# Performance work log

Measured on AMD Instinct MI355X. Metric: run time of the kernel, lower is better.

The kernel has to match this reference:

```python
import jax, jax.numpy as jnp
import numpy as np

B, C, S = 16, 8, 128
DT, DX, DY = 0.001, 1.0, 1.0
NUM_STEPS = 10
EPS = 1e-6


def _thomas(a, b, c, d):
    """Batched Thomas tridiagonal solve. a,b,c,d: [M,N] rows; solve along N."""
    aT, bT, cT, dT = a.T, b.T, c.T, d.T  # [N, M]
    zero = jnp.zeros_like(dT[0])

    def fwd(carry, inp):
        cs_p, ds_p = carry
        ai, bi, ci, di = inp
        denom = bi - ai * cs_p + EPS  # i=0: cs_p=0 -> denom = b0 + eps (matches torch)
        cs = ci / denom
        ds = (di - ai * ds_p) / denom
        return (cs, ds), (cs, ds)

    _, (c_star, d_star) = jax.lax.scan(fwd, (zero, zero), (aT, bT, cT, dT))

    def bwd(x_next, inp):
        ci, di = inp
        x = di - ci * x_next
        return x, x

    _, xs = jax.lax.scan(bwd, d_star[-1], (c_star[:-1], d_star[:-1]), reverse=True)
    x = jnp.concatenate([xs, d_star[-1:]], axis=0)  # [N, M]
    return x.T


def _diffuse_rows(u2d, coeff):
    """Implicit 1D diffusion along last axis. u2d, coeff: [M,N]."""
    a = -coeff
    c = -coeff
    b = 1.0 + 2.0 * coeff
    b = b.at[:, 0].set(1.0 + coeff[:, 0])
    b = b.at[:, -1].set(1.0 + coeff[:, -1])
    return _thomas(a, b, c, u2d)


def _forward(u, alpha_base, beta_base, alpha_time_coeff, beta_time_coeff, channel_mixing):
    Bb, Cc, H, W = u.shape
    half = DT / 2.0
    t = 0.0
    for _ in range(NUM_STEPS):
        # x half-step (coefficient alpha at time t)
        alpha = jnp.clip(alpha_base + alpha_time_coeff * t, EPS, 10.0)
        u = jnp.einsum('dc,bchw->bdhw', channel_mixing, u)
        uf = u.reshape(Bb * Cc, H, W)
        af = jnp.broadcast_to(alpha[None], (Bb, Cc, H, W)).reshape(Bb * Cc, H, W)
        uf = _diffuse_rows(uf.reshape(-1, W), af.reshape(-1, W) * half / DX**2).reshape(Bb * Cc, H, W)
        t += half
        # y full step (coefficient beta at time t+dt/2)
        beta = jnp.clip(beta_base + beta_time_coeff * t, EPS, 10.0)
        bf = jnp.broadcast_to(beta[None], (Bb, Cc, H, W)).reshape(Bb * Cc, H, W)
        ut = uf.transpose(0, 2, 1).reshape(-1, H)
        bt = bf.transpose(0, 2, 1).reshape(-1, H)
        ut = _diffuse_rows(ut, bt * DT / DY**2)
        uf = ut.reshape(Bb * Cc, W, H).transpose(0, 2, 1)
        t += half
        # x half-step (coefficient alpha at time t+dt)
        alpha = jnp.clip(alpha_base + alpha_time_coeff * t, EPS, 10.0)
        af = jnp.broadcast_to(alpha[None], (Bb, Cc, H, W)).reshape(Bb * Cc, H, W)
        uf = _diffuse_rows(uf.reshape(-1, W), af.reshape(-1, W) * half / DX**2).reshape(Bb * Cc, H, W)
        u = uf.reshape(Bb, Cc, H, W)
    return u


def setup_inputs() -> dict:
    key = jax.random.key(0)
    k_u, k_cm, k_atc, k_btc = jax.random.split(key, 4)
    u = jax.random.normal(k_u, (B, C, S, S), dtype=jnp.float32)
    alpha_base = jnp.ones((C, S, S), dtype=jnp.float32)
    beta_base = jnp.ones((C, S, S), dtype=jnp.float32)
    alpha_time_coeff = jax.random.normal(k_atc, (C, S, S), dtype=jnp.float32) * 0.01
    beta_time_coeff = jax.random.normal(k_btc, (C, S, S), dtype=jnp.float32) * 0.01
    channel_mixing = jnp.eye(C, dtype=jnp.float32) + jax.random.normal(k_cm, (C, C), dtype=jnp.float32) * 0.01
    return {
        'u': u,
        'alpha_base': alpha_base,
        'beta_base': beta_base,
        'alpha_time_coeff': alpha_time_coeff,
        'beta_time_coeff': beta_time_coeff,
        'channel_mixing': channel_mixing,
    }


def reference(u, alpha_base, beta_base, alpha_time_coeff, beta_time_coeff, channel_mixing):
    return _forward(u, alpha_base, beta_base, alpha_time_coeff, beta_time_coeff, channel_mixing)
```

## Files before the change

### kernel.cpp

```cpp
#include <hip/hip_runtime.h>
#include <hip/hip_fp16.h>


constexpr int S_  = 128;
constexpr int RS  = 129;
constexpr float EPSF = 1e-6f;
constexpr int CSS = 8 * 128 * 128;

constexpr int SOFF_A = 0;
constexpr int SOFF_B = 64 * 128;
constexpr int SOFF_C = 128 * 128;
constexpr int SPOOL  = 192 * 128;

__device__ __forceinline__ int swad(int r, int b) {
    return r * 128 + (((b) ^ (r & 31)) << 2);
}

template <int N>
__device__ __forceinline__ void jrunN(const float (&e)[N], const float (&g)[N],
                                      float (&o)[N - 4]) {
    float x1[N];
    #pragma unroll
    for (int i = 1; i <= N - 2; ++i) x1[i] = fmaf(g[i], e[i - 1] + e[i + 1], e[i]);
    #pragma unroll
    for (int i = 2; i <= N - 3; ++i) o[i - 2] = fmaf(g[i], x1[i - 1] + x1[i + 1], e[i]);
}

__global__ __launch_bounds__(256) void coef_kernel(
    const float* __restrict__ ab, const float* __restrict__ atc,
    const float* __restrict__ bb, const float* __restrict__ btc,
    __half2* __restrict__ cf)
{
    for (int gc = blockIdx.x * 256 + threadIdx.x; gc < CSS; gc += gridDim.x * 256) {
        const int w = gc & 127, h = (gc >> 7) & 127;
        const float abv = ab[gc], atv = atc[gc], bbv = bb[gc], btv = btc[gc];
        const float nbY = (h == 0 || h == S_ - 1) ? 1.f : 2.f;
        const float nbX = (w == 0 || w == S_ - 1) ? 1.f : 2.f;
        for (int k = 0; k < 10; ++k) {
            const float ty = (2 * k + 1) * 0.0005f;
            const float tx = (2 * k + 2) * 0.0005f;
            float be = fminf(fmaxf(fmaf(btv, ty, bbv), EPSF), 10.f);
            float co = be * 0.001f;
            float rb = __builtin_amdgcn_rcpf(fmaf(nbY, co, 1.f) + EPSF);
            cf[k * CSS + gc] = __floats2half2_rn(rb * co, rb - 1.f);
            float al = fminf(fmaxf(fmaf(atv, tx, abv), EPSF), 10.f);
            co = al * 0.0005f;
            rb = __builtin_amdgcn_rcpf(fmaf(nbX, co, 1.f) + EPSF);
            cf[(10 + k) * CSS + gc] = __floats2half2_rn(rb * co, rb - 1.f);
        }
        float al = fminf(fmaxf(abv, EPSF), 10.f);
        float co = al * 0.0005f;
        float rb = __builtin_amdgcn_rcpf(fmaf(nbX, co, 1.f) + EPSF);
        cf[20 * CSS + gc] = __floats2half2_rn(rb * co, rb - 1.f);
    }
}

__global__ __launch_bounds__(512, 2) void head_kernel(
    const float* __restrict__ u0, __half* __restrict__ ud,
    const __half2* __restrict__ cfy, const __half2* __restrict__ cfx,
    const __half2* __restrict__ cfx0, const float* __restrict__ cm)
{
    constexpr int POOL   = 288 * RS;
    constexpr int OFF_A  = 0;
    constexpr int OFF_B  = 64 * RS;
    constexpr int OFF_CP = 192 * RS;
    constexpr int OFF_X0 = 96 * RS;
    __shared__ float sP[POOL];
    const int tid = threadIdx.x;
    const int b   = blockIdx.x >> 4;
    const int h0  = (blockIdx.x & 15) << 3;

    #pragma unroll
    for (int m = 0; m < 2; ++m) {
        const int col = tid + 512 * m;
        const int c = col >> 7, w = col & 127;
        #pragma unroll
        for (int hh = 0; hh < 12; ++hh) {
            const int gh = h0 - 2 + hh;
            float v = 0.f;
            if (gh >= 0 && gh < S_) v = u0[((b * 8 + c) * S_ + gh) * S_ + w];
            sP[(c * 12 + hh) * RS + w] = v;
        }
    }
    #pragma unroll
    for (int m = 0; m < 12; ++m) {
        const int task = tid + 512 * m;
        const int r = task >> 6, col2 = task & 63;
        const int c = r / 12, hh = r % 12;
        int gh = h0 - 2 + hh; gh = gh < 0 ? 0 : (gh >= S_ ? S_ - 1 : gh);
        const uint2 v = ((const uint2*)cfx0)[(c * S_ + gh) * 64 + col2];
        sP[OFF_CP + r * RS + col2 * 2]     = __uint_as_float(v.x);
        sP[OFF_CP + r * RS + col2 * 2 + 1] = __uint_as_float(v.y);
    }
    __syncthreads();
    {
        float M[64];
        #pragma unroll
        for (int i = 0; i < 64; ++i) M[i] = cm[i];
        #pragma unroll
        for (int m = 0; m < 3; ++m) {
            const int p = tid + 512 * m;
            const int hh = p >> 7, w = p & 127;
            float v[8], o[8];
            #pragma unroll
            for (int c = 0; c < 8; ++c) v[c] = sP[(c * 12 + hh) * RS + w];
            #pragma unroll
            for (int dd = 0; dd < 8; ++dd) {
                float a = 0.f;
                #pragma unroll
                for (int c = 0; c < 8; ++c) a = fmaf(M[dd * 8 + c], v[c], a);
                o[dd] = a;
            }
            #pragma unroll
            for (int c = 0; c < 8; ++c) sP[(c * 12 + hh) * RS + w] = o[c];
        }
    }
    __syncthreads();
    #pragma unroll
    for (int m = 0; m < 3; ++m) {
        const int task = tid + 512 * m;
        const int r96 = task % 96, wr = task / 96;
        const int hh = r96 % 12;
        const int gh = h0 - 2 + hh;
        const bool rowin = (gh >= 0 && gh < S_);
        const int w0 = wr * 8;
        float e[12], g[12];
        #pragma unroll
        for (int j = 0; j < 12; ++j) {
            const int wj = w0 - 2 + j;
            const bool win = (wj >= 0 && wj < S_);
            const float dv = win ? sP[r96 * RS + wj] : 0.f;
            uint cb = (rowin && win) ? __float_as_uint(sP[OFF_CP + r96 * RS + wj]) : 0u;
            const float2 f = __half22float2(*reinterpret_cast<__half2*>(&cb));
            e[j] = (1.f + f.y) * dv;
            g[j] = f.x;
        }
        float o[8]; jrunN<12>(e, g, o);
        #pragma unroll
        for (int i = 0; i < 8; ++i) sP[OFF_X0 + r96 * RS + w0 + i] = o[i];
    }
    __syncthreads();

    #pragma unroll
    for (int m = 0; m < 2; ++m) {
        const int col = tid + 512 * m;
        const int c = col >> 7, w = col & 127;
        float e[12], g[12];
        #pragma unroll
        for (int hh = 0; hh < 12; ++hh) {
            const int gh = h0 - 2 + hh;
            const bool inr = (gh >= 0 && gh < S_);
            const int ghc = inr ? gh : 0;
            const float dv = sP[OFF_X0 + (c * 12 + hh) * RS + w];
            const float2 f = __half22float2(cfy[(c * S_ + ghc) * S_ + w]);
            e[hh] = (1.f + f.y) * dv;
            g[hh] = inr ? f.x : 0.f;
        }
        float o[8]; jrunN<12>(e, g, o);
        #pragma unroll
        for (int i = 0; i < 8; ++i) sP[OFF_A + (c * 8 + i) * RS + w] = o[i];
    }
    __syncthreads();
    #pragma unroll
    for (int m = 0; m < 8; ++m) {
        const int task = tid + 512 * m;
        const int r = task >> 6, col2 = task & 63;
        const int c = r >> 3, ho = r & 7;
        const uint2 v = ((const uint2*)cfx)[(c * S_ + h0 + ho) * 64 + col2];
        sP[OFF_CP + r * RS + col2 * 2]     = __uint_as_float(v.x);
        sP[OFF_CP + r * RS + col2 * 2 + 1] = __uint_as_float(v.y);
    }
    __syncthreads();

    float rbk[2][12], gk[2][12], xo[2][8];
    #pragma unroll
    for (int m = 0; m < 2; ++m) {
        const int run = tid + 512 * m;
        const int r = run & 63, wr = run >> 6;
        const int w0 = wr * 8;
        float e[12];
        #pragma unroll
        for (int j = 0; j < 12; ++j) {
            const int wj = w0 - 2 + j;
            const bool win = (wj >= 0 && wj < S_);
            const float dv = win ? sP[OFF_A + r * RS + wj] : 0.f;
            uint cb = win ? __float_as_uint(sP[OFF_CP + r * RS + wj]) : 0u;
            const float2 f = __half22float2(*reinterpret_cast<__half2*>(&cb));
            rbk[m][j] = 1.f + f.y; gk[m][j] = f.x;
            e[j] = rbk[m][j] * dv;
        }
        jrunN<12>(e, gk[m], xo[m]);
    }
    #pragma unroll
    for (int m = 0; m < 2; ++m) {
        const int run = tid + 512 * m;
        const int r = run & 63, w0 = (run >> 6) * 8;
        #pragma unroll
        for (int i = 0; i < 8; ++i) sP[OFF_B + r * RS + w0 + i] = xo[m][i];
    }
    __syncthreads();
    {
        float M[64];
        #pragma unroll
        for (int i = 0; i < 64; ++i) M[i] = cm[i];
        #pragma unroll
        for (int m = 0; m < 2; ++m) {
            const int p = tid + 512 * m;
            const int ho = p >> 7, w = p & 127;
            float v[8], o[8];
            #pragma unroll
            for (int c = 0; c < 8; ++c) v[c] = sP[OFF_B + (c * 8 + ho) * RS + w];
            #pragma unroll
            for (int dd = 0; dd < 8; ++dd) {
                float a = 0.f;
                #pragma unroll
                for (int c = 0; c < 8; ++c) a = fmaf(M[dd * 8 + c], v[c], a);
                o[dd] = a;
            }
            #pragma unroll
            for (int c = 0; c < 8; ++c) sP[OFF_A + (c * 8 + ho) * RS + w] = o[c];
        }
    }
    __syncthreads();
    #pragma unroll
    for (int m = 0; m < 2; ++m) {
        const int run = tid + 512 * m;
        const int r = run & 63, wr = run >> 6;
        const int w0 = wr * 8;
        const int c = r >> 3, ho = r & 7;
        float e[12];
        #pragma unroll
        for (int j = 0; j < 12; ++j) {
            const int wj = w0 - 2 + j;
            const bool win = (wj >= 0 && wj < S_);
            const float dv = win ? sP[OFF_A + r * RS + wj] : 0.f;
            e[j] = rbk[m][j] * dv;
        }
        float o[8]; jrunN<12>(e, gk[m], o);
        __half2* d2 = (__half2*)&ud[((b * 8 + c) * S_ + h0 + ho) * S_ + w0];
        d2[0] = __floats2half2_rn(o[0], o[1]);
        d2[1] = __floats2half2_rn(o[2], o[3]);
        d2[2] = __floats2half2_rn(o[4], o[5]);
        d2[3] = __floats2half2_rn(o[6], o[7]);
    }
}

template <bool LASTK>
__global__ __launch_bounds__(512) void stepS_kernel(
    const __half* __restrict__ us, void* __restrict__ udst_,
    const __half2* __restrict__ cfy, const __half2* __restrict__ cfx,
    const float* __restrict__ cm)
{
    __shared__ __align__(16) float sP[SPOOL];
    const int tid = threadIdx.x;
    const int b   = blockIdx.x >> 4;
    const int h0  = (blockIdx.x & 15) << 3;

    {
        const int c  = tid >> 6;
        const int wp = tid & 63;
        const int wbase = 2 * wp;
        uint du[12]; uint2 dc[12];
        #pragma unroll
        for (int hh = 0; hh < 12; ++hh) {
            const int gh = h0 - 2 + hh;
            const bool inr = (gh >= 0 && gh < S_);
            const int ghc = inr ? gh : 0;
            du[hh] = inr ? *(const uint*)&us[((b * 8 + c) * S_ + ghc) * S_ + wbase] : 0u;
            dc[hh] = *(const uint2*)&cfy[(c * S_ + ghc) * S_ + wbase];
        }
        float o2[2][8];
        #pragma unroll
        for (int s = 0; s < 2; ++s) {
            float e[12], g[12];
            #pragma unroll
            for (int hh = 0; hh < 12; ++hh) {
                const int gh = h0 - 2 + hh;
                const bool inr = (gh >= 0 && gh < S_);
                uint ub = du[hh];
                __half2 hu = *reinterpret_cast<__half2*>(&ub);
                const float dv = s ? __high2float(hu) : __low2float(hu);
                uint cb = s ? dc[hh].y : dc[hh].x;
                const float2 f = __half22float2(*reinterpret_cast<__half2*>(&cb));
                e[hh] = (1.f + f.y) * dv;
                g[hh] = inr ? f.x : 0.f;
            }
            jrunN<12>(e, g, o2[s]);
        }
        #pragma unroll
        for (int i = 0; i < 8; ++i) {
            const int r = c * 8 + i;
            float2* p = (float2*)&sP[SOFF_A + r * 128 +
                                     (((wp >> 1) ^ (r & 31)) << 2) + 2 * (wp & 1)];
            *p = make_float2(o2[0][i], o2[1][i]);
        }
    }
    {
        const uint* cfxu = (const uint*)cfx;
        #pragma unroll
        for (int m = 0; m < 4; ++m) {
            const int task = tid + 512 * m;
            const int r = task >> 5, col4 = task & 31;
            const int c = r >> 3, ho = r & 7;
            const uint4 v = *(const uint4*)&cfxu[(c * S_ + h0 + ho) * S_ + col4 * 4];
            *(float4*)&sP[SOFF_C + swad(r, col4)] =
                make_float4(__uint_as_float(v.x), __uint_as_float(v.y),
                            __uint_as_float(v.z), __uint_as_float(v.w));
        }
    }
    __syncthreads();

    float rbk[2][12], gk[2][12], xo[2][8];
    #pragma unroll
    for (int m = 0; m < 2; ++m) {
        const int r  = tid & 63;
        const int wr = (tid >> 6) + 8 * m;
        const int w0 = wr * 8;
        float f[16]; uint cb[16];
        #pragma unroll
        for (int i = 0; i < 4; ++i) {
            const int bb = (w0 >> 2) - 1 + i;
            if (bb >= 0 && bb < 32) {
                const float4 va = *(const float4*)&sP[SOFF_A + swad(r, bb)];
                const float4 vc = *(const float4*)&sP[SOFF_C + swad(r, bb)];
                f[4 * i + 0] = va.x; f[4 * i + 1] = va.y;
                f[4 * i + 2] = va.z; f[4 * i + 3] = va.w;
                cb[4 * i + 0] = __float_as_uint(vc.x);
                cb[4 * i + 1] = __float_as_uint(vc.y);
                cb[4 * i + 2] = __float_as_uint(vc.z);
                cb[4 * i + 3] = __float_as_uint(vc.w);
            } else {
                f[4 * i + 0] = f[4 * i + 1] = f[4 * i + 2] = f[4 * i + 3] = 0.f;
                cb[4 * i + 0] = cb[4 * i + 1] = cb[4 * i + 2] = cb[4 * i + 3] = 0u;
            }
        }
        float e[12];
        #pragma unroll
        for (int j = 0; j < 12; ++j) {
            uint c_ = cb[j + 2];
            const float2 fc = __half22float2(*reinterpret_cast<__half2*>(&c_));
            rbk[m][j] = 1.f + fc.y; gk[m][j] = fc.x;
            e[j] = rbk[m][j] * f[j + 2];
        }
        jrunN<12>(e, gk[m], xo[m]);
    }

    if (LASTK) {
        float* ud = (float*)udst_;
        #pragma unroll
        for (int m = 0; m < 2; ++m) {
            const int r  = tid & 63;
            const int wr = (tid >> 6) + 8 * m;
            const int c = r >> 3, ho = r & 7;
            float4* dst4 = (float4*)&ud[((b * 8 + c) * S_ + h0 + ho) * S_ + wr * 8];
            dst4[0] = make_float4(xo[m][0], xo[m][1], xo[m][2], xo[m][3]);
            dst4[1] = make_float4(xo[m][4], xo[m][5], xo[m][6], xo[m][7]);
        }
    } else {
        #pragma unroll
        for (int m = 0; m < 2; ++m) {
            const int r  = tid & 63;
            const int wr = (tid >> 6) + 8 * m;
            *(float4*)&sP[SOFF_B + swad(r, 2 * wr)] =
                make_float4(xo[m][0], xo[m][1], xo[m][2], xo[m][3]);
            *(float4*)&sP[SOFF_B + swad(r, 2 * wr + 1)] =
                make_float4(xo[m][4], xo[m][5], xo[m][6], xo[m][7]);
        }
        __syncthreads();
        {
            float M[64];
            #pragma unroll
            for (int i = 0; i < 64; ++i) M[i] = cm[i];
            #pragma unroll
            for (int m = 0; m < 2; ++m) {
                const int p = tid + 512 * m;
                const int ho = p >> 7, w = p & 127;
                float v[8], o[8];
                #pragma unroll
                for (int c = 0; c < 8; ++c) {
                    const int r = c * 8 + ho;
                    v[c] = sP[SOFF_B + r * 128 + (((w >> 2) ^ (r & 31)) << 2) + (w & 3)];
                }
                #pragma unroll
                for (int dd = 0; dd < 8; ++dd) {
                    float a = 0.f;
                    #pragma unroll
                    for (int c = 0; c < 8; ++c) a = fmaf(M[dd * 8 + c], v[c], a);
                    o[dd] = a;
                }
                #pragma unroll
                for (int c = 0; c < 8; ++c) {
                    const int r = c * 8 + ho;
                    sP[SOFF_A + r * 128 + (((w >> 2) ^ (r & 31)) << 2) + (w & 3)] = o[c];
                }
            }
        }
        __syncthreads();
        __half* ud = (__half*)udst_;
        #pragma unroll
        for (int m = 0; m < 2; ++m) {
            const int r  = tid & 63;
            const int wr = (tid >> 6) + 8 * m;
            const int w0 = wr * 8;
            const int c = r >> 3, ho = r & 7;
            float f[16];
            #pragma unroll
            for (int i = 0; i < 4; ++i) {
                const int bb = (w0 >> 2) - 1 + i;
                if (bb >= 0 && bb < 32) {
                    const float4 va = *(const float4*)&sP[SOFF_A + swad(r, bb)];
                    f[4 * i + 0] = va.x; f[4 * i + 1] = va.y;
                    f[4 * i + 2] = va.z; f[4 * i + 3] = va.w;
                } else {
                    f[4 * i + 0] = f[4 * i + 1] = f[4 * i + 2] = f[4 * i + 3] = 0.f;
                }
            }
            float e[12];
            #pragma unroll
            for (int j = 0; j < 12; ++j) e[j] = rbk[m][j] * f[j + 2];
            float o[8]; jrunN<12>(e, gk[m], o);
            __half2 q0 = __floats2half2_rn(o[0], o[1]);
            __half2 q1 = __floats2half2_rn(o[2], o[3]);
            __half2 q2 = __floats2half2_rn(o[4], o[5]);
            __half2 q3 = __floats2half2_rn(o[6], o[7]);
            uint4 pk;
            pk.x = *reinterpret_cast<uint*>(&q0);
            pk.y = *reinterpret_cast<uint*>(&q1);
            pk.z = *reinterpret_cast<uint*>(&q2);
            pk.w = *reinterpret_cast<uint*>(&q3);
            *(uint4*)&ud[((b * 8 + c) * S_ + h0 + ho) * S_ + w0] = pk;
        }
    }
}

extern "C" void kernel_launch(void* const* d_in, const int* in_sizes, int n_in,
                              void* d_out, int out_size, void* d_ws, size_t ws_size,
                              hipStream_t stream) {
    const float* u_in = (const float*)d_in[0];
    const float* ab   = (const float*)d_in[1];
    const float* bbta = (const float*)d_in[2];
    const float* atc  = (const float*)d_in[3];
    const float* btc  = (const float*)d_in[4];
    const float* cm   = (const float*)d_in[5];
    float* uo = (float*)d_out;
    __half*  h1 = (__half*)d_ws;
    __half*  h2 = (__half*)((char*)d_ws + (8u << 20));
    __half2* cf = (__half2*)((char*)d_ws + (16u << 20));

    coef_kernel<<<dim3(512), dim3(256), 0, stream>>>(ab, atc, bbta, btc, cf);

    const dim3 g(256), blk(512);
    head_kernel<<<g, blk, 0, stream>>>(u_in, h1, cf + 0 * CSS, cf + 10 * CSS,
                                       cf + 20 * CSS, cm);
    const __half* s = h1; __half* d = h2;
    for (int k = 1; k <= 8; ++k) {
        stepS_kernel<false><<<g, blk, 0, stream>>>(s, d, cf + k * CSS,
                                                   cf + (10 + k) * CSS, cm);
        const __half* ns = d;
        d = (d == h2) ? h1 : h2;
        s = ns;
    }
    stepS_kernel<true><<<g, blk, 0, stream>>>(s, uo, cf + 9 * CSS,
                                              cf + 19 * CSS, cm);
}
```

Baseline: 152.7 us.

## Store single half coefficient per cell and recompute rb; swizzle head kernel LDS

The coefficient table now stores only g=rb*co as one half per cell instead of a half2 (g, rb-1). The kernels rebuild rb as 1-nb*g, which halves coefficient traffic in every step kernel. The head kernel computes its first x-step coefficients directly from alpha_base and moves to the XOR-swizzled float4 LDS layout, with vectorised loads and less shared memory, dropping the min-2-blocks launch bound. The cost is a few extra FMAs per tap and a small precision change from deriving rb out of the rounded g.

```diff
diff --git a/kernel.cpp b/kernel.cpp
--- a/kernel.cpp
+++ b/kernel.cpp
@@ -3,17 +3,24 @@
 
 
 constexpr int S_  = 128;
-constexpr int RS  = 129;
 constexpr float EPSF = 1e-6f;
 constexpr int CSS = 8 * 128 * 128;
 
-constexpr int SOFF_A = 0;
-constexpr int SOFF_B = 64 * 128;
-constexpr int SOFF_C = 128 * 128;
-constexpr int SPOOL  = 192 * 128;
-
-__device__ __forceinline__ int swad(int r, int b) {
-    return r * 128 + (((b) ^ (r & 31)) << 2);
+constexpr int SA = 0;
+constexpr int SB = 64 * 128;
+constexpr int SC = 128 * 128;
+constexpr int SPOOL = 192 * 128;
+constexpr int HA  = 0;
+constexpr int HST = 96 * 128;
+constexpr int HB  = 96 * 128;
+constexpr int HC  = 192 * 128;
+constexpr int HPOOL = 256 * 128;
+
+__device__ __forceinline__ int swad4(int r, int b4) {
+    return r * 128 + (((b4) ^ (r & 31)) << 2);
+}
+__device__ __forceinline__ int swadw(int r, int w) {
+    return r * 128 + ((((w) >> 2) ^ (r & 31)) << 2) + ((w) & 3);
 }
 
 template <int N>
@@ -26,71 +33,66 @@
     for (int i = 2; i <= N - 3; ++i) o[i - 2] = fmaf(g[i], x1[i - 1] + x1[i + 1], e[i]);
 }
 
+#define TAPS2(RA, RC, f, gt)                                                   \
+    {                                                                          \
+        _Pragma("unroll")                                                      \
+        for (int i_ = 0; i_ < 4; ++i_) {                                       \
+            const int bb_ = 2 * wr - 1 + i_;                                   \
+            if (bb_ >= 0 && bb_ < 32) {                                        \
+                const float4 va_ = *(const float4*)&sP[(RA) + swad4(r, bb_)];  \
+                const float4 vc_ = *(const float4*)&sP[(RC) + swad4(r, bb_)];  \
+                f[4*i_+0]=va_.x; f[4*i_+1]=va_.y; f[4*i_+2]=va_.z; f[4*i_+3]=va_.w; \
+                gt[4*i_+0]=vc_.x; gt[4*i_+1]=vc_.y; gt[4*i_+2]=vc_.z; gt[4*i_+3]=vc_.w; \
+            } else {                                                           \
+                f[4*i_+0]=f[4*i_+1]=f[4*i_+2]=f[4*i_+3]=0.f;                   \
+                gt[4*i_+0]=gt[4*i_+1]=gt[4*i_+2]=gt[4*i_+3]=0.f;               \
+            }                                                                  \
+        }                                                                      \
+    }
+
 __global__ __launch_bounds__(256) void coef_kernel(
     const float* __restrict__ ab, const float* __restrict__ atc,
     const float* __restrict__ bb, const float* __restrict__ btc,
-    __half2* __restrict__ cf)
+    __half* __restrict__ cg)
 {
     for (int gc = blockIdx.x * 256 + threadIdx.x; gc < CSS; gc += gridDim.x * 256) {
         const int w = gc & 127, h = (gc >> 7) & 127;
         const float abv = ab[gc], atv = atc[gc], bbv = bb[gc], btv = btc[gc];
         const float nbY = (h == 0 || h == S_ - 1) ? 1.f : 2.f;
         const float nbX = (w == 0 || w == S_ - 1) ? 1.f : 2.f;
+        #pragma unroll
         for (int k = 0; k < 10; ++k) {
-            const float ty = (2 * k + 1) * 0.0005f;
-            const float tx = (2 * k + 2) * 0.0005f;
-            float be = fminf(fmaxf(fmaf(btv, ty, bbv), EPSF), 10.f);
+            float be = fminf(fmaxf(fmaf(btv, (2 * k + 1) * 0.0005f, bbv), EPSF), 10.f);
             float co = be * 0.001f;
             float rb = __builtin_amdgcn_rcpf(fmaf(nbY, co, 1.f) + EPSF);
-            cf[k * CSS + gc] = __floats2half2_rn(rb * co, rb - 1.f);
-            float al = fminf(fmaxf(fmaf(atv, tx, abv), EPSF), 10.f);
+            cg[k * CSS + gc] = __float2half(rb * co);
+            float al = fminf(fmaxf(fmaf(atv, (2 * k + 2) * 0.0005f, abv), EPSF), 10.f);
             co = al * 0.0005f;
             rb = __builtin_amdgcn_rcpf(fmaf(nbX, co, 1.f) + EPSF);
-            cf[(10 + k) * CSS + gc] = __floats2half2_rn(rb * co, rb - 1.f);
-        }
-        float al = fminf(fmaxf(abv, EPSF), 10.f);
-        float co = al * 0.0005f;
-        float rb = __builtin_amdgcn_rcpf(fmaf(nbX, co, 1.f) + EPSF);
-        cf[20 * CSS + gc] = __floats2half2_rn(rb * co, rb - 1.f);
-    }
-}
-
-__global__ __launch_bounds__(512, 2) void head_kernel(
+            cg[(10 + k) * CSS + gc] = __float2half(rb * co);
+        }
+    }
+}
+
+__global__ __launch_bounds__(512) void head_kernel(
     const float* __restrict__ u0, __half* __restrict__ ud,
-    const __half2* __restrict__ cfy, const __half2* __restrict__ cfx,
-    const __half2* __restrict__ cfx0, const float* __restrict__ cm)
+    const float* __restrict__ ab, const __half* __restrict__ cgy,
+    const __half* __restrict__ cgx, const float* __restrict__ cm)
 {
-    constexpr int POOL   = 288 * RS;
-    constexpr int OFF_A  = 0;
-    constexpr int OFF_B  = 64 * RS;
-    constexpr int OFF_CP = 192 * RS;
-    constexpr int OFF_X0 = 96 * RS;
-    __shared__ float sP[POOL];
+    __shared__ __align__(16) float sP[HPOOL];
     const int tid = threadIdx.x;
     const int b   = blockIdx.x >> 4;
     const int h0  = (blockIdx.x & 15) << 3;
 
     #pragma unroll
-    for (int m = 0; m < 2; ++m) {
-        const int col = tid + 512 * m;
-        const int c = col >> 7, w = col & 127;
-        #pragma unroll
-        for (int hh = 0; hh < 12; ++hh) {
-            const int gh = h0 - 2 + hh;
-            float v = 0.f;
-            if (gh >= 0 && gh < S_) v = u0[((b * 8 + c) * S_ + gh) * S_ + w];
-            sP[(c * 12 + hh) * RS + w] = v;
-        }
-    }
-    #pragma unroll
-    for (int m = 0; m < 12; ++m) {
+    for (int m = 0; m < 6; ++m) {
         const int task = tid + 512 * m;
-        const int r = task >> 6, col2 = task & 63;
-        const int c = r / 12, hh = r % 12;
-        int gh = h0 - 2 + hh; gh = gh < 0 ? 0 : (gh >= S_ ? S_ - 1 : gh);
-        const uint2 v = ((const uint2*)cfx0)[(c * S_ + gh) * 64 + col2];
-        sP[OFF_CP + r * RS + col2 * 2]     = __uint_as_float(v.x);
-        sP[OFF_CP + r * RS + col2 * 2 + 1] = __uint_as_float(v.y);
+        const int r = task >> 5, b4 = task & 31;
+        const int c = r / 12, hh = r - c * 12;
+        const int gh = h0 - 2 + hh;
+        float4 v = make_float4(0.f, 0.f, 0.f, 0.f);
+        if (gh >= 0 && gh < S_) v = *(const float4*)&u0[((b * 8 + c) * S_ + gh) * S_ + 4 * b4];
+        *(float4*)&sP[HST + swad4(r, b4)] = v;
     }
     __syncthreads();
     {
@@ -103,7 +105,7 @@
             const int hh = p >> 7, w = p & 127;
             float v[8], o[8];
             #pragma unroll
-            for (int c = 0; c < 8; ++c) v[c] = sP[(c * 12 + hh) * RS + w];
+            for (int c = 0; c < 8; ++c) v[c] = sP[HST + swadw(c * 12 + hh, w)];
             #pragma unroll
             for (int dd = 0; dd < 8; ++dd) {
                 float a = 0.f;
@@ -112,91 +114,137 @@
                 o[dd] = a;
             }
             #pragma unroll
-            for (int c = 0; c < 8; ++c) sP[(c * 12 + hh) * RS + w] = o[c];
-        }
-    }
-    __syncthreads();
-    #pragma unroll
-    for (int m = 0; m < 3; ++m) {
-        const int task = tid + 512 * m;
-        const int r96 = task % 96, wr = task / 96;
-        const int hh = r96 % 12;
-        const int gh = h0 - 2 + hh;
-        const bool rowin = (gh >= 0 && gh < S_);
-        const int w0 = wr * 8;
-        float e[12], g[12];
-        #pragma unroll
-        for (int j = 0; j < 12; ++j) {
-            const int wj = w0 - 2 + j;
-            const bool win = (wj >= 0 && wj < S_);
-            const float dv = win ? sP[r96 * RS + wj] : 0.f;
-            uint cb = (rowin && win) ? __float_as_uint(sP[OFF_CP + r96 * RS + wj]) : 0u;
-            const float2 f = __half22float2(*reinterpret_cast<__half2*>(&cb));
-            e[j] = (1.f + f.y) * dv;
-            g[j] = f.x;
-        }
-        float o[8]; jrunN<12>(e, g, o);
-        #pragma unroll
-        for (int i = 0; i < 8; ++i) sP[OFF_X0 + r96 * RS + w0 + i] = o[i];
-    }
-    __syncthreads();
-
-    #pragma unroll
-    for (int m = 0; m < 2; ++m) {
-        const int col = tid + 512 * m;
-        const int c = col >> 7, w = col & 127;
-        float e[12], g[12];
+            for (int c = 0; c < 8; ++c) sP[HST + swadw(c * 12 + hh, w)] = o[c];
+        }
+    }
+    __syncthreads();
+    {
+        float xh[3][8];
+        #pragma unroll
+        for (int m = 0; m < 3; ++m) {
+            const int r  = (tid & 31) + 32 * m;
+            const int wr = tid >> 5;
+            const int w0 = wr * 8;
+            const int c = r / 12, hh = r - c * 12;
+            const int gh = h0 - 2 + hh;
+            const bool rowin = (gh >= 0 && gh < S_);
+            float f[16];
+            #pragma unroll
+            for (int i = 0; i < 4; ++i) {
+                const int bb4 = 2 * wr - 1 + i;
+                if (bb4 >= 0 && bb4 < 32) {
+                    const float4 va = *(const float4*)&sP[HST + swad4(r, bb4)];
+                    f[4*i+0]=va.x; f[4*i+1]=va.y; f[4*i+2]=va.z; f[4*i+3]=va.w;
+                } else {
+                    f[4*i+0]=f[4*i+1]=f[4*i+2]=f[4*i+3]=0.f;
+                }
+            }
+            float e[12], g[12];
+            #pragma unroll
+            for (int j = 0; j < 12; ++j) {
+                const int wj = w0 - 2 + j;
+                const bool win = (wj >= 0 && wj < S_);
+                float co = 0.f;
+                if (rowin && win) {
+                    float al = ab[(c * S_ + gh) * S_ + wj];
+                    co = fminf(fmaxf(al, EPSF), 10.f) * 0.0005f;
+                }
+                const float nb = (wj == 0 || wj == S_ - 1) ? 1.f : 2.f;
+                const float rb = __builtin_amdgcn_rcpf(fmaf(nb, co, 1.f) + EPSF);
+                e[j] = rb * f[j + 2]; g[j] = rb * co;
+            }
+            jrunN<12>(e, g, xh[m]);
+        }
+        __syncthreads();
+        #pragma unroll
+        for (int m = 0; m < 3; ++m) {
+            const int r  = (tid & 31) + 32 * m;
+            const int wr = tid >> 5;
+            *(float4*)&sP[HST + swad4(r, 2 * wr)]     = make_float4(xh[m][0], xh[m][1], xh[m][2], xh[m][3]);
+            *(float4*)&sP[HST + swad4(r, 2 * wr + 1)] = make_float4(xh[m][4], xh[m][5], xh[m][6], xh[m][7]);
+        }
+    }
+    __syncthreads();
+    {
+        const int c = tid >> 6, wp = tid & 63, wb = 2 * wp;
+        float2 dp[12]; uint dg[12];
         #pragma unroll
         for (int hh = 0; hh < 12; ++hh) {
             const int gh = h0 - 2 + hh;
             const bool inr = (gh >= 0 && gh < S_);
             const int ghc = inr ? gh : 0;
-            const float dv = sP[OFF_X0 + (c * 12 + hh) * RS + w];
-            const float2 f = __half22float2(cfy[(c * S_ + ghc) * S_ + w]);
-            e[hh] = (1.f + f.y) * dv;
-            g[hh] = inr ? f.x : 0.f;
-        }
-        float o[8]; jrunN<12>(e, g, o);
-        #pragma unroll
-        for (int i = 0; i < 8; ++i) sP[OFF_A + (c * 8 + i) * RS + w] = o[i];
-    }
-    __syncthreads();
-    #pragma unroll
-    for (int m = 0; m < 8; ++m) {
-        const int task = tid + 512 * m;
-        const int r = task >> 6, col2 = task & 63;
-        const int c = r >> 3, ho = r & 7;
-        const uint2 v = ((const uint2*)cfx)[(c * S_ + h0 + ho) * 64 + col2];
-        sP[OFF_CP + r * RS + col2 * 2]     = __uint_as_float(v.x);
-        sP[OFF_CP + r * RS + col2 * 2 + 1] = __uint_as_float(v.y);
-    }
-    __syncthreads();
-
+            const int r = c * 12 + hh;
+            dp[hh] = *(const float2*)&sP[HST + r * 128 +
+                                         (((wp >> 1) ^ (r & 31)) << 2) + 2 * (wp & 1)];
+            dg[hh] = *(const uint*)&cgy[(c * S_ + ghc) * S_ + wb];
+        }
+        float o2[2][8];
+        #pragma unroll
+        for (int s = 0; s < 2; ++s) {
+            float e[12], g[12];
+            #pragma unroll
+            for (int hh = 0; hh < 12; ++hh) {
+                const int gh = h0 - 2 + hh;
+                const bool inr = (gh >= 0 && gh < S_);
+                uint gb = dg[hh];
+                __half2 hg = *reinterpret_cast<__half2*>(&gb);
+                float gv = s ? __high2float(hg) : __low2float(hg);
+                gv = inr ? gv : 0.f;
+                const float nb = (gh == 0 || gh == S_ - 1) ? 1.f : 2.f;
+                const float rb = fmaf(-nb, gv, 1.f);
+                e[hh] = rb * (s ? dp[hh].y : dp[hh].x);
+                g[hh] = gv;
+            }
+            jrunN<12>(e, g, o2[s]);
+        }
+        #pragma unroll
+        for (int i = 0; i < 8; ++i) {
+            const int r = c * 8 + i;
+            *(float2*)&sP[HA + r * 128 + (((wp >> 1) ^ (r & 31)) << 2) + 2 * (wp & 1)]
+                = make_float2(o2[0][i], o2[1][i]);
+        }
+    }
+    {
+        const ushort* cx = (const ushort*)cgx;
+        #pragma unroll
+        for (int m = 0; m < 4; ++m) {
+            const int task = tid + 512 * m;
+            const int r = task >> 5, b4 = task & 31;
+            const int c = r >> 3, ho = r & 7;
+            const uint2 v = *(const uint2*)&cx[(c * S_ + h0 + ho) * S_ + b4 * 4];
+            uint lo = v.x, hi = v.y;
+            __half2 h0_ = *reinterpret_cast<__half2*>(&lo);
+            __half2 h1_ = *reinterpret_cast<__half2*>(&hi);
+            *(float4*)&sP[HC + swad4(r, b4)] = make_float4(
+                __low2float(h0_), __high2float(h0_), __low2float(h1_), __high2float(h1_));
+        }
+    }
+    __syncthreads();
     float rbk[2][12], gk[2][12], xo[2][8];
     #pragma unroll
     for (int m = 0; m < 2; ++m) {
-        const int run = tid + 512 * m;
-        const int r = run & 63, wr = run >> 6;
+        const int r  = tid & 63;
+        const int wr = (tid >> 6) + 8 * m;
         const int w0 = wr * 8;
+        float f[16], gt[16];
+        TAPS2(HA, HC, f, gt)
         float e[12];
         #pragma unroll
         for (int j = 0; j < 12; ++j) {
             const int wj = w0 - 2 + j;
-            const bool win = (wj >= 0 && wj < S_);
-            const float dv = win ? sP[OFF_A + r * RS + wj] : 0.f;
-            uint cb = win ? __float_as_uint(sP[OFF_CP + r * RS + wj]) : 0u;
-            const float2 f = __half22float2(*reinterpret_cast<__half2*>(&cb));
-            rbk[m][j] = 1.f + f.y; gk[m][j] = f.x;
-            e[j] = rbk[m][j] * dv;
+            const float nb = (wj == 0 || wj == S_ - 1) ? 1.f : 2.f;
+            gk[m][j] = gt[j + 2];
+            rbk[m][j] = fmaf(-nb, gt[j + 2], 1.f);
+            e[j] = rbk[m][j] * f[j + 2];
         }
         jrunN<12>(e, gk[m], xo[m]);
     }
     #pragma unroll
     for (int m = 0; m < 2; ++m) {
-        const int run = tid + 512 * m;
-        const int r = run & 63, w0 = (run >> 6) * 8;
-        #pragma unroll
-        for (int i = 0; i < 8; ++i) sP[OFF_B + r * RS + w0 + i] = xo[m][i];
+        const int r  = tid & 63;
+        const int wr = (tid >> 6) + 8 * m;
+        *(float4*)&sP[HB + swad4(r, 2 * wr)]     = make_float4(xo[m][0], xo[m][1], xo[m][2], xo[m][3]);
+        *(float4*)&sP[HB + swad4(r, 2 * wr + 1)] = make_float4(xo[m][4], xo[m][5], xo[m][6], xo[m][7]);
     }
     __syncthreads();
     {
@@ -209,7 +257,7 @@
             const int ho = p >> 7, w = p & 127;
             float v[8], o[8];
             #pragma unroll
-            for (int c = 0; c < 8; ++c) v[c] = sP[OFF_B + (c * 8 + ho) * RS + w];
+            for (int c = 0; c < 8; ++c) v[c] = sP[HB + swadw(c * 8 + ho, w)];
             #pragma unroll
             for (int dd = 0; dd < 8; ++dd) {
                 float a = 0.f;
@@ -218,37 +266,47 @@
                 o[dd] = a;
             }
             #pragma unroll
-            for (int c = 0; c < 8; ++c) sP[OFF_A + (c * 8 + ho) * RS + w] = o[c];
+            for (int c = 0; c < 8; ++c) sP[HA + swadw(c * 8 + ho, w)] = o[c];
         }
     }
     __syncthreads();
     #pragma unroll
     for (int m = 0; m < 2; ++m) {
-        const int run = tid + 512 * m;
-        const int r = run & 63, wr = run >> 6;
-        const int w0 = wr * 8;
+        const int r  = tid & 63;
+        const int wr = (tid >> 6) + 8 * m;
         const int c = r >> 3, ho = r & 7;
+        float f[16];
+        #pragma unroll
+        for (int i = 0; i < 4; ++i) {
+            const int bb4 = 2 * wr - 1 + i;
+            if (bb4 >= 0 && bb4 < 32) {
+                const float4 va = *(const float4*)&sP[HA + swad4(r, bb4)];
+                f[4*i+0]=va.x; f[4*i+1]=va.y; f[4*i+2]=va.z; f[4*i+3]=va.w;
+            } else {
+                f[4*i+0]=f[4*i+1]=f[4*i+2]=f[4*i+3]=0.f;
+            }
+        }
         float e[12];
         #pragma unroll
-        for (int j = 0; j < 12; ++j) {
-            const int wj = w0 - 2 + j;
-            const bool win = (wj >= 0 && wj < S_);
-            const float dv = win ? sP[OFF_A + r * RS + wj] : 0.f;
-            e[j] = rbk[m][j] * dv;
-        }
+        for (int j = 0; j < 12; ++j) e[j] = rbk[m][j] * f[j + 2];
         float o[8]; jrunN<12>(e, gk[m], o);
-        __half2* d2 = (__half2*)&ud[((b * 8 + c) * S_ + h0 + ho) * S_ + w0];
-        d2[0] = __floats2half2_rn(o[0], o[1]);
-        d2[1] = __floats2half2_rn(o[2], o[3]);
-        d2[2] = __floats2half2_rn(o[4], o[5]);
-        d2[3] = __floats2half2_rn(o[6], o[7]);
+        __half2 q0 = __floats2half2_rn(o[0], o[1]);
+        __half2 q1 = __floats2half2_rn(o[2], o[3]);
+        __half2 q2 = __floats2half2_rn(o[4], o[5]);
+        __half2 q3 = __floats2half2_rn(o[6], o[7]);
+        uint4 pk;
+        pk.x = *reinterpret_cast<uint*>(&q0);
+        pk.y = *reinterpret_cast<uint*>(&q1);
+        pk.z = *reinterpret_cast<uint*>(&q2);
+        pk.w = *reinterpret_cast<uint*>(&q3);
+        *(uint4*)&ud[((b * 8 + c) * S_ + h0 + ho) * S_ + wr * 8] = pk;
     }
 }
 
 template <bool LASTK>
 __global__ __launch_bounds__(512) void stepS_kernel(
     const __half* __restrict__ us, void* __restrict__ udst_,
-    const __half2* __restrict__ cfy, const __half2* __restrict__ cfx,
+    const __half* __restrict__ cgy, const __half* __restrict__ cgx,
     const float* __restrict__ cm)
 {
     __shared__ __align__(16) float sP[SPOOL];
@@ -257,17 +315,15 @@
     const int h0  = (blockIdx.x & 15) << 3;
 
     {
-        const int c  = tid >> 6;
-        const int wp = tid & 63;
-        const int wbase = 2 * wp;
-        uint du[12]; uint2 dc[12];
+        const int c = tid >> 6, wp = tid & 63, wb = 2 * wp;
+        uint du[12], dg[12];
         #pragma unroll
         for (int hh = 0; hh < 12; ++hh) {
             const int gh = h0 - 2 + hh;
             const bool inr = (gh >= 0 && gh < S_);
             const int ghc = inr ? gh : 0;
-            du[hh] = inr ? *(const uint*)&us[((b * 8 + c) * S_ + ghc) * S_ + wbase] : 0u;
-            dc[hh] = *(const uint2*)&cfy[(c * S_ + ghc) * S_ + wbase];
+            du[hh] = inr ? *(const uint*)&us[((b * 8 + c) * S_ + ghc) * S_ + wb] : 0u;
+            dg[hh] = *(const uint*)&cgy[(c * S_ + ghc) * S_ + wb];
         }
         float o2[2][8];
         #pragma unroll
@@ -280,32 +336,37 @@
                 uint ub = du[hh];
                 __half2 hu = *reinterpret_cast<__half2*>(&ub);
                 const float dv = s ? __high2float(hu) : __low2float(hu);
-                uint cb = s ? dc[hh].y : dc[hh].x;
-                const float2 f = __half22float2(*reinterpret_cast<__half2*>(&cb));
-                e[hh] = (1.f + f.y) * dv;
-                g[hh] = inr ? f.x : 0.f;
+                uint gb = dg[hh];
+                __half2 hg = *reinterpret_cast<__half2*>(&gb);
+                float gv = s ? __high2float(hg) : __low2float(hg);
+                gv = inr ? gv : 0.f;
+                const float nb = (gh == 0 || gh == S_ - 1) ? 1.f : 2.f;
+                const float rb = fmaf(-nb, gv, 1.f);
+                e[hh] = rb * dv;
+                g[hh] = gv;
             }
             jrunN<12>(e, g, o2[s]);
         }
         #pragma unroll
         for (int i = 0; i < 8; ++i) {
             const int r = c * 8 + i;
-            float2* p = (float2*)&sP[SOFF_A + r * 128 +
-                                     (((wp >> 1) ^ (r & 31)) << 2) + 2 * (wp & 1)];
-            *p = make_float2(o2[0][i], o2[1][i]);
-        }
-    }
-    {
-        const uint* cfxu = (const uint*)cfx;
+            *(float2*)&sP[SA + r * 128 + (((wp >> 1) ^ (r & 31)) << 2) + 2 * (wp & 1)]
+                = make_float2(o2[0][i], o2[1][i]);
+        }
+    }
+    {
+        const ushort* cx = (const ushort*)cgx;
         #pragma unroll
         for (int m = 0; m < 4; ++m) {
             const int task = tid + 512 * m;
-            const int r = task >> 5, col4 = task & 31;
+            const int r = task >> 5, b4 = task & 31;
             const int c = r >> 3, ho = r & 7;
-            const uint4 v = *(const uint4*)&cfxu[(c * S_ + h0 + ho) * S_ + col4 * 4];
-            *(float4*)&sP[SOFF_C + swad(r, col4)] =
-                make_float4(__uint_as_float(v.x), __uint_as_float(v.y),
-                            __uint_as_float(v.z), __uint_as_float(v.w));
+            const uint2 v = *(const uint2*)&cx[(c * S_ + h0 + ho) * S_ + b4 * 4];
+            uint lo = v.x, hi = v.y;
+            __half2 h0_ = *reinterpret_cast<__half2*>(&lo);
+            __half2 h1_ = *reinterpret_cast<__half2*>(&hi);
+            *(float4*)&sP[SC + swad4(r, b4)] = make_float4(
+                __low2float(h0_), __high2float(h0_), __low2float(h1_), __high2float(h1_));
         }
     }
     __syncthreads();
@@ -316,30 +377,15 @@
         const int r  = tid & 63;
         const int wr = (tid >> 6) + 8 * m;
         const int w0 = wr * 8;
-        float f[16]; uint cb[16];
-        #pragma unroll
-        for (int i = 0; i < 4; ++i) {
-            const int bb = (w0 >> 2) - 1 + i;
-            if (bb >= 0 && bb < 32) {
-                const float4 va = *(const float4*)&sP[SOFF_A + swad(r, bb)];
-                const float4 vc = *(const float4*)&sP[SOFF_C + swad(r, bb)];
-                f[4 * i + 0] = va.x; f[4 * i + 1] = va.y;
-                f[4 * i + 2] = va.z; f[4 * i + 3] = va.w;
-                cb[4 * i + 0] = __float_as_uint(vc.x);
-                cb[4 * i + 1] = __float_as_uint(vc.y);
-                cb[4 * i + 2] = __float_as_uint(vc.z);
-                cb[4 * i + 3] = __float_as_uint(vc.w);
-            } else {
-                f[4 * i + 0] = f[4 * i + 1] = f[4 * i + 2] = f[4 * i + 3] = 0.f;
-                cb[4 * i + 0] = cb[4 * i + 1] = cb[4 * i + 2] = cb[4 * i + 3] = 0u;
-            }
-        }
+        float f[16], gt[16];
+        TAPS2(SA, SC, f, gt)
         float e[12];
         #pragma unroll
         for (int j = 0; j < 12; ++j) {
-            uint c_ = cb[j + 2];
-            const float2 fc = __half22float2(*reinterpret_cast<__half2*>(&c_));
-            rbk[m][j] = 1.f + fc.y; gk[m][j] = fc.x;
+            const int wj = w0 - 2 + j;
+            const float nb = (wj == 0 || wj == S_ - 1) ? 1.f : 2.f;
+            gk[m][j] = gt[j + 2];
+            rbk[m][j] = fmaf(-nb, gt[j + 2], 1.f);
             e[j] = rbk[m][j] * f[j + 2];
         }
         jrunN<12>(e, gk[m], xo[m]);
@@ -361,10 +407,8 @@
         for (int m = 0; m < 2; ++m) {
             const int r  = tid & 63;
             const int wr = (tid >> 6) + 8 * m;
-            *(float4*)&sP[SOFF_B + swad(r, 2 * wr)] =
-                make_float4(xo[m][0], xo[m][1], xo[m][2], xo[m][3]);
-            *(float4*)&sP[SOFF_B + swad(r, 2 * wr + 1)] =
-                make_float4(xo[m][4], xo[m][5], xo[m][6], xo[m][7]);
+            *(float4*)&sP[SB + swad4(r, 2 * wr)]     = make_float4(xo[m][0], xo[m][1], xo[m][2], xo[m][3]);
+            *(float4*)&sP[SB + swad4(r, 2 * wr + 1)] = make_float4(xo[m][4], xo[m][5], xo[m][6], xo[m][7]);
         }
         __syncthreads();
         {
@@ -377,10 +421,7 @@
                 const int ho = p >> 7, w = p & 127;
                 float v[8], o[8];
                 #pragma unroll
-                for (int c = 0; c < 8; ++c) {
-                    const int r = c * 8 + ho;
-                    v[c] = sP[SOFF_B + r * 128 + (((w >> 2) ^ (r & 31)) << 2) + (w & 3)];
-                }
+                for (int c = 0; c < 8; ++c) v[c] = sP[SB + swadw(c * 8 + ho, w)];
                 #pragma unroll
                 for (int dd = 0; dd < 8; ++dd) {
                     float a = 0.f;
@@ -389,10 +430,7 @@
                     o[dd] = a;
                 }
                 #pragma unroll
-                for (int c = 0; c < 8; ++c) {
-                    const int r = c * 8 + ho;
-                    sP[SOFF_A + r * 128 + (((w >> 2) ^ (r & 31)) << 2) + (w & 3)] = o[c];
-                }
+                for (int c = 0; c < 8; ++c) sP[SA + swadw(c * 8 + ho, w)] = o[c];
             }
         }
         __syncthreads();
@@ -401,18 +439,16 @@
         for (int m = 0; m < 2; ++m) {
             const int r  = tid & 63;
             const int wr = (tid >> 6) + 8 * m;
-            const int w0 = wr * 8;
             const int c = r >> 3, ho = r & 7;
             float f[16];
             #pragma unroll
             for (int i = 0; i < 4; ++i) {
-                const int bb = (w0 >> 2) - 1 + i;
-                if (bb >= 0 && bb < 32) {
-                    const float4 va = *(const float4*)&sP[SOFF_A + swad(r, bb)];
-                    f[4 * i + 0] = va.x; f[4 * i + 1] = va.y;
-                    f[4 * i + 2] = va.z; f[4 * i + 3] = va.w;
+                const int bb4 = 2 * wr - 1 + i;
+                if (bb4 >= 0 && bb4 < 32) {
+                    const float4 va = *(const float4*)&sP[SA + swad4(r, bb4)];
+                    f[4*i+0]=va.x; f[4*i+1]=va.y; f[4*i+2]=va.z; f[4*i+3]=va.w;
                 } else {
-                    f[4 * i + 0] = f[4 * i + 1] = f[4 * i + 2] = f[4 * i + 3] = 0.f;
+                    f[4*i+0]=f[4*i+1]=f[4*i+2]=f[4*i+3]=0.f;
                 }
             }
             float e[12];
@@ -428,7 +464,7 @@
             pk.y = *reinterpret_cast<uint*>(&q1);
             pk.z = *reinterpret_cast<uint*>(&q2);
             pk.w = *reinterpret_cast<uint*>(&q3);
-            *(uint4*)&ud[((b * 8 + c) * S_ + h0 + ho) * S_ + w0] = pk;
+            *(uint4*)&ud[((b * 8 + c) * S_ + h0 + ho) * S_ + wr * 8] = pk;
         }
     }
 }
@@ -443,23 +479,23 @@
     const float* btc  = (const float*)d_in[4];
     const float* cm   = (const float*)d_in[5];
     float* uo = (float*)d_out;
-    __half*  h1 = (__half*)d_ws;
-    __half*  h2 = (__half*)((char*)d_ws + (8u << 20));
-    __half2* cf = (__half2*)((char*)d_ws + (16u << 20));
-
-    coef_kernel<<<dim3(512), dim3(256), 0, stream>>>(ab, atc, bbta, btc, cf);
+    __half* h1 = (__half*)d_ws;
+    __half* h2 = (__half*)((char*)d_ws + (8u << 20));
+    __half* cg = (__half*)((char*)d_ws + (16u << 20));
+
+    coef_kernel<<<dim3(512), dim3(256), 0, stream>>>(ab, atc, bbta, btc, cg);
 
     const dim3 g(256), blk(512);
-    head_kernel<<<g, blk, 0, stream>>>(u_in, h1, cf + 0 * CSS, cf + 10 * CSS,
-                                       cf + 20 * CSS, cm);
+    head_kernel<<<g, blk, 0, stream>>>(u_in, h1, ab, cg + 0 * CSS,
+                                       cg + 10 * CSS, cm);
     const __half* s = h1; __half* d = h2;
     for (int k = 1; k <= 8; ++k) {
-        stepS_kernel<false><<<g, blk, 0, stream>>>(s, d, cf + k * CSS,
-                                                   cf + (10 + k) * CSS, cm);
+        stepS_kernel<false><<<g, blk, 0, stream>>>(s, d, cg + k * CSS,
+                                                   cg + (10 + k) * CSS, cm);
         const __half* ns = d;
         d = (d == h2) ? h1 : h2;
         s = ns;
     }
-    stepS_kernel<true><<<g, blk, 0, stream>>>(s, uo, cf + 9 * CSS,
-                                              cf + 19 * CSS, cm);
-}
+    stepS_kernel<true><<<g, blk, 0, stream>>>(s, uo, cg + 9 * CSS,
+                                              cg + 19 * CSS, cm);
+}
```

Measured after the change: 156.1 us. +2.2%, slower.
